# Performance work log

Measured on AMD Instinct MI355X. Metric: run time of the kernel, lower is better.

Reference implementation:

```python
import jax, jax.numpy as jnp
import numpy as np

IN_DIM, K, D, ITERS, EPS = 512, 8, 128, 3, 1e-8
LN_EPS = 1e-5

def _ln(x, g, b):
    m = jnp.mean(x, axis=-1, keepdims=True)
    v = jnp.var(x, axis=-1, keepdims=True)
    return (x - m) * jax.lax.rsqrt(v + LN_EPS) * g + b

def setup_inputs() -> dict:
    key = jax.random.key(0)
    ks = jax.random.split(key, 16)
    B, C, H, W = 64, IN_DIM, 32, 32
    s = lambda fan: 1.0 / np.sqrt(fan)
    inp = {
        'x': jax.random.normal(ks[0], (B, C, H, W), jnp.float32),
        'noise': jax.random.normal(ks[1], (B, K, D), jnp.float32),
        'slot_mu': jax.random.normal(ks[2], (1, K, D), jnp.float32) * 0.02,
        'slot_log_sigma': jnp.zeros((1, K, D), jnp.float32),
        'Wp': jax.random.uniform(ks[3], (IN_DIM, D), jnp.float32, -s(IN_DIM), s(IN_DIM)),
        'bp': jnp.zeros((D,), jnp.float32),
        'g_in': jnp.ones((D,), jnp.float32), 'b_in': jnp.zeros((D,), jnp.float32),
        'Wq': jax.random.uniform(ks[4], (D, D), jnp.float32, -s(D), s(D)),
        'bq': jnp.zeros((D,), jnp.float32),
        'Wk': jax.random.uniform(ks[5], (D, D), jnp.float32, -s(D), s(D)),
        'bk': jnp.zeros((D,), jnp.float32),
        'Wv': jax.random.uniform(ks[6], (D, D), jnp.float32, -s(D), s(D)),
        'bv': jnp.zeros((D,), jnp.float32),
        'W_ih': jax.random.uniform(ks[7], (3 * D, D), jnp.float32, -s(D), s(D)),
        'W_hh': jax.random.uniform(ks[8], (3 * D, D), jnp.float32, -s(D), s(D)),
        'b_ih': jax.random.uniform(ks[9], (3 * D,), jnp.float32, -s(D), s(D)),
        'b_hh': jax.random.uniform(ks[10], (3 * D,), jnp.float32, -s(D), s(D)),
        'W1': jax.random.uniform(ks[11], (D, 2 * D), jnp.float32, -s(D), s(D)),
        'b1': jnp.zeros((2 * D,), jnp.float32),
        'W2': jax.random.uniform(ks[12], (2 * D, D), jnp.float32, -s(2 * D), s(2 * D)),
        'b2': jnp.zeros((D,), jnp.float32),
        'g_slots': jnp.ones((D,), jnp.float32), 'b_slots': jnp.zeros((D,), jnp.float32),
        'g_mlp': jnp.ones((D,), jnp.float32), 'b_mlp': jnp.zeros((D,), jnp.float32),
    }
    return inp

def reference(x, noise, slot_mu, slot_log_sigma, Wp, bp, g_in, b_in,
              Wq, bq, Wk, bk, Wv, bv, W_ih, W_hh, b_ih, b_hh,
              W1, b1, W2, b2, g_slots, b_slots, g_mlp, b_mlp):
    B, C, H, W = x.shape
    N = H * W
    scale = D ** -0.5
    x_flat = x.reshape(B, C, N).transpose(0, 2, 1)          # [B,N,C]
    inputs = _ln(x_flat @ Wp + bp, g_in, b_in)              # [B,N,D]
    slots = slot_mu + jnp.exp(slot_log_sigma) * noise       # [B,K,D]
    k = inputs @ Wk + bk                                    # k/v are loop-invariant
    v = inputs @ Wv + bv
    attn = None
    for _ in range(ITERS):
        slots_prev = slots
        q = _ln(slots, g_slots, b_slots) @ Wq + bq          # [B,K,D]
        logits = jnp.einsum('bkd,bnd->bkn', q, k) * scale
        attn = jax.nn.softmax(logits, axis=1)               # softmax over slots
        attn_norm = attn / (jnp.sum(attn, axis=-1, keepdims=True) + EPS)
        updates = jnp.einsum('bkn,bnd->bkd', attn_norm, v)  # [B,K,D]
        # GRUCell (PyTorch gate order r,z,n)
        u2 = updates.reshape(B * K, D)
        h = slots_prev.reshape(B * K, D)
        gx = u2 @ W_ih.T + b_ih
        gh = h @ W_hh.T + b_hh
        xr, xz, xn = jnp.split(gx, 3, axis=-1)
        hr, hz, hn = jnp.split(gh, 3, axis=-1)
        r = jax.nn.sigmoid(xr + hr)
        z = jax.nn.sigmoid(xz + hz)
        n = jnp.tanh(xn + r * hn)
        slots = ((1.0 - z) * n + z * h).reshape(B, K, D)
        hmid = jax.nn.gelu(_ln(slots, g_mlp, b_mlp) @ W1 + b1, approximate=False)
        slots = slots + hmid @ W2 + b2
    return slots, attn
```

## Files before the change

kernel.cpp:

```cpp
#include <hip/hip_runtime.h>
#include <hip/hip_bf16.h>
#include <math.h>

#define B_ 64
#define C_ 512
#define N_ 1024
#define D_ 128
#define K_ 8

typedef __attribute__((ext_vector_type(8))) short bf16x8;
typedef __attribute__((ext_vector_type(4))) float f32x4;
typedef unsigned short ushort_t;

__device__ __forceinline__ unsigned short f2bs(float f) {
    union { __hip_bfloat16 h; unsigned short s; } u;
    u.h = __float2bfloat16(f);
    return u.s;
}
__device__ __forceinline__ float bs2f(unsigned short s) {
    union { unsigned int u; float f; } v;
    v.u = ((unsigned int)s) << 16;
    return v.f;
}
__device__ __forceinline__ float sigmoidf_(float x) { return 1.0f / (1.0f + expf(-x)); }
__device__ __forceinline__ float gelu_exact(float x) {
    return 0.5f * x * (1.0f + erff(x * 0.7071067811865476f));
}

__global__ __launch_bounds__(256) void prep_init(
    const float* __restrict__ Wp, const float* __restrict__ Wk,
    const float* __restrict__ Wv, const float* __restrict__ W_ih,
    const float* __restrict__ W_hh,
    const float* __restrict__ noise, const float* __restrict__ mu,
    const float* __restrict__ lsig,
    const float* __restrict__ g_slots, const float* __restrict__ b_slots,
    const float* __restrict__ Wq, const float* __restrict__ bq,
    ushort_t* __restrict__ WpT, ushort_t* __restrict__ WkT,
    ushort_t* __restrict__ WvT, float* __restrict__ WTih,
    float* __restrict__ WThh,
    float* __restrict__ slots, float* __restrict__ qbuf)
{
    __shared__ float sl2[2][128];
    __shared__ float tt2[2][128];
    __shared__ float mrs2[2][2];
    const int t = threadIdx.x;

    if (blockIdx.x < 256) {
        int tid = blockIdx.x * 256 + t;
        {
            int c = tid >> 7, d = tid & 127;
            WpT[d * 512 + c] = f2bs(Wp[tid]);
        }
        if (tid < 16384) {
            int c = tid >> 7, d = tid & 127;
            WkT[d * 128 + c] = f2bs(Wk[tid]);
            WvT[d * 128 + c] = f2bs(Wv[tid]);
        }
        if (tid < 49152) {
            int j = tid >> 7, c = tid & 127;
            WTih[c * 384 + j] = W_ih[tid];
            WThh[c * 384 + j] = W_hh[tid];
        }
        return;
    }

    const int lr = t >> 7, lt = t & 127;
    const int row = ((blockIdx.x - 256) << 1) | lr;
    const int b = row >> 3;
    const int kd = (row & 7) * 128 + lt;
    float sv = mu[kd] + expf(lsig[kd]) * noise[b * 1024 + kd];
    slots[(size_t)row * D_ + lt] = sv;
    sl2[lr][lt] = sv;
    __syncthreads();
    if (lt < 64) {
        float v0 = sl2[lr][lt], v1 = sl2[lr][lt + 64];
        float s = v0 + v1, s2 = v0 * v0 + v1 * v1;
        for (int off = 32; off > 0; off >>= 1) {
            s += __shfl_down(s, off, 64);
            s2 += __shfl_down(s2, off, 64);
        }
        if (lt == 0) {
            float mean = s * (1.f / 128.f);
            float var = s2 * (1.f / 128.f) - mean * mean;
            mrs2[lr][0] = mean; mrs2[lr][1] = rsqrtf(var + 1e-5f);
        }
    }
    __syncthreads();
    tt2[lr][lt] = (sl2[lr][lt] - mrs2[lr][0]) * mrs2[lr][1] * g_slots[lt] + b_slots[lt];
    __syncthreads();
    float a = bq[lt];
    for (int c = 0; c < 128; ++c) a = fmaf(tt2[lr][c], Wq[(size_t)c * D_ + lt], a);
    qbuf[(size_t)row * D_ + lt] = a;
}

__global__ __launch_bounds__(256) void proj_kv(
    const float* __restrict__ x, const ushort_t* __restrict__ WpT,
    const float* __restrict__ bp, const float* __restrict__ g_in,
    const float* __restrict__ b_in,
    const ushort_t* __restrict__ WkT, const float* __restrict__ bk,
    const ushort_t* __restrict__ WvT, const float* __restrict__ bv,
    ushort_t* __restrict__ kout, ushort_t* __restrict__ vout)
{
    __shared__ __align__(16) ushort_t Al[64 * 40];
    __shared__ __align__(16) ushort_t Bl[128 * 40];
    __shared__ __align__(16) ushort_t Bv2[128 * 40];
    __shared__ __align__(16) ushort_t A2[64 * 136];
    __shared__ float red[64][2][2];
    const int t = threadIdx.x;
    const int b = blockIdx.x >> 4;
    const int n0 = (blockIdx.x & 15) << 6;
    const int w = t >> 6, lane = t & 63;
    const int quad = lane >> 4, m = lane & 15;
    const int rowoff = (w >> 1) << 5;
    const int coloff = (w & 1) << 6;

    f32x4 acc[2][4];
#pragma unroll
    for (int r = 0; r < 2; ++r)
#pragma unroll
        for (int c = 0; c < 4; ++c) acc[r][c] = (f32x4){0.f, 0.f, 0.f, 0.f};

    const float* xb = x + (size_t)b * (C_ * N_);
    for (int c0 = 0; c0 < C_; c0 += 32) {
#pragma unroll
        for (int i = 0; i < 2; ++i) {
            int idx = t + (i << 8);
            int cc = idx >> 4;
            int nn4 = (idx & 15) << 2;
            float4 xv = *(const float4*)&xb[(size_t)(c0 + cc) * N_ + n0 + nn4];
            Al[(nn4    ) * 40 + cc] = f2bs(xv.x);
            Al[(nn4 + 1) * 40 + cc] = f2bs(xv.y);
            Al[(nn4 + 2) * 40 + cc] = f2bs(xv.z);
            Al[(nn4 + 3) * 40 + cc] = f2bs(xv.w);
        }
#pragma unroll
        for (int i = 0; i < 2; ++i) {
            int idx = t + (i << 8);
            int d = idx >> 2, seg = idx & 3;
            *(bf16x8*)&Bl[d * 40 + seg * 8] =
                *(const bf16x8*)&WpT[d * 512 + c0 + seg * 8];
        }
        __syncthreads();
        bf16x8 af[2], bfr[4];
#pragma unroll
        for (int r = 0; r < 2; ++r)
            af[r] = *(const bf16x8*)&Al[(rowoff + 16 * r + m) * 40 + quad * 8];
#pragma unroll
        for (int c = 0; c < 4; ++c)
            bfr[c] = *(const bf16x8*)&Bl[(coloff + 16 * c + m) * 40 + quad * 8];
#pragma unroll
        for (int r = 0; r < 2; ++r)
#pragma unroll
            for (int c = 0; c < 4; ++c)
                acc[r][c] = __builtin_amdgcn_mfma_f32_16x16x32_bf16(af[r], bfr[c], acc[r][c], 0, 0, 0);
        __syncthreads();
    }
    float gv[4], bvv[4], bpv[4];
#pragma unroll
    for (int c = 0; c < 4; ++c) {
        int col = coloff + 16 * c + m;
        bpv[c] = bp[col]; gv[c] = g_in[col]; bvv[c] = b_in[col];
    }
#pragma unroll
    for (int r = 0; r < 2; ++r)
#pragma unroll
        for (int c = 0; c < 4; ++c)
#pragma unroll
            for (int g = 0; g < 4; ++g) acc[r][c][g] += bpv[c];

#pragma unroll
    for (int r = 0; r < 2; ++r) {
#pragma unroll
        for (int g = 0; g < 4; ++g) {
            float s = 0.f, s2 = 0.f;
#pragma unroll
            for (int c = 0; c < 4; ++c) { float v = acc[r][c][g]; s += v; s2 += v * v; }
#pragma unroll
            for (int off = 1; off < 16; off <<= 1) {
                s += __shfl_xor(s, off, 64);
                s2 += __shfl_xor(s2, off, 64);
            }
            if (m == 0) {
                int row = rowoff + 16 * r + quad * 4 + g;
                red[row][w & 1][0] = s;
                red[row][w & 1][1] = s2;
            }
        }
    }
    __syncthreads();
#pragma unroll
    for (int r = 0; r < 2; ++r) {
#pragma unroll
        for (int g = 0; g < 4; ++g) {
            int row = rowoff + 16 * r + quad * 4 + g;
            float s = red[row][0][0] + red[row][1][0];
            float s2 = red[row][0][1] + red[row][1][1];
            float mean = s * (1.f / 128.f);
            float var = s2 * (1.f / 128.f) - mean * mean;
            float rs = rsqrtf(var + 1e-5f);
#pragma unroll
            for (int c = 0; c < 4; ++c) {
                int col = coloff + 16 * c + m;
                float v = (acc[r][c][g] - mean) * rs * gv[c] + bvv[c];
                A2[row * 136 + col] = f2bs(v);
            }
        }
    }

    const int is_v = w >> 1;
    const int rowoff2 = (w & 1) << 5;
    f32x4 acc2[2][8];
#pragma unroll
    for (int r = 0; r < 2; ++r)
#pragma unroll
        for (int c = 0; c < 8; ++c) acc2[r][c] = (f32x4){0.f, 0.f, 0.f, 0.f};

    for (int c0 = 0; c0 < D_; c0 += 32) {
#pragma unroll
        for (int i = 0; i < 2; ++i) {
            int idx = t + (i << 8);
            int d = idx >> 2, seg = idx & 3;
            *(bf16x8*)&Bl[d * 40 + seg * 8] =
                *(const bf16x8*)&WkT[d * 128 + c0 + seg * 8];
            *(bf16x8*)&Bv2[d * 40 + seg * 8] =
                *(const bf16x8*)&WvT[d * 128 + c0 + seg * 8];
        }
        __syncthreads();
        const ushort_t* Bsrc = is_v ? Bv2 : Bl;
        bf16x8 af[2], bfr[8];
#pragma unroll
        for (int r = 0; r < 2; ++r)
            af[r] = *(const bf16x8*)&A2[(rowoff2 + 16 * r + m) * 136 + c0 + quad * 8];
#pragma unroll
        for (int c = 0; c < 8; ++c)
            bfr[c] = *(const bf16x8*)&Bsrc[(16 * c + m) * 40 + quad * 8];
#pragma unroll
        for (int r = 0; r < 2; ++r)
#pragma unroll
            for (int c = 0; c < 8; ++c)
                acc2[r][c] = __builtin_amdgcn_mfma_f32_16x16x32_bf16(af[r], bfr[c], acc2[r][c], 0, 0, 0);
        __syncthreads();
    }
    const float* bias = is_v ? bv : bk;
    ushort_t* dst = is_v ? vout : kout;
    float bval[8];
#pragma unroll
    for (int c = 0; c < 8; ++c) bval[c] = bias[16 * c + m];
#pragma unroll
    for (int r = 0; r < 2; ++r) {
#pragma unroll
        for (int g = 0; g < 4; ++g) {
            int row = rowoff2 + 16 * r + quad * 4 + g;
            size_t base = ((size_t)b * N_ + n0 + row) * D_;
#pragma unroll
            for (int c = 0; c < 8; ++c)
                dst[base + 16 * c + m] = f2bs(acc2[r][c][g] + bval[c]);
        }
    }
}

__global__ __launch_bounds__(512, 2) void attn_pv(
    const ushort_t* __restrict__ kb, const ushort_t* __restrict__ vb,
    const float* __restrict__ qbuf,
    float* __restrict__ S_part, float* __restrict__ upd_part,
    float* __restrict__ out_attn, int last)
{
    __shared__ __align__(16) char scratch[69632];
    __shared__ __align__(16) float at8[8][264];
    __shared__ __align__(16) float qs[8][132];
    __shared__ float red2[4][8];
    ushort_t* kvt = (ushort_t*)scratch;
    float* red = (float*)scratch;

    const int t = threadIdx.x;
    const int qd = blockIdx.x, b = blockIdx.y;
    const int nbase = qd << 8;
    const int wv = t >> 6, lane = t & 63;
    const float SCALE = 0.08838834764831845f;

    for (int i = t; i < 1024; i += 512)
        qs[i >> 7][i & 127] = qbuf[(size_t)b * 1024 + i];
#pragma unroll
    for (int i = 0; i < 8; ++i) {
        int idx = t + (i << 9);
        int rr = idx >> 4, u8 = (idx & 15) << 3;
        *(bf16x8*)&kvt[rr * 136 + u8] =
            *(const bf16x8*)&kb[((size_t)b * N_ + nbase + rr) * D_ + u8];
    }
    __syncthreads();

    {
        const int rr = t & 255, kh = t >> 8;
        float acc[4] = {0.f, 0.f, 0.f, 0.f};
        for (int c0 = 0; c0 < 128; c0 += 8) {
            bf16x8 kr = *(const bf16x8*)&kvt[rr * 136 + c0];
            float kf[8];
#pragma unroll
            for (int j = 0; j < 8; ++j) kf[j] = bs2f((ushort_t)kr[j]);
#pragma unroll
            for (int kk = 0; kk < 4; ++kk) {
                f32x4 qa = *(const f32x4*)&qs[4 * kh + kk][c0];
                f32x4 qb = *(const f32x4*)&qs[4 * kh + kk][c0 + 4];
                acc[kk] = fmaf(qa[0], kf[0], acc[kk]);
                acc[kk] = fmaf(qa[1], kf[1], acc[kk]);
                acc[kk] = fmaf(qa[2], kf[2], acc[kk]);
                acc[kk] = fmaf(qa[3], kf[3], acc[kk]);
                acc[kk] = fmaf(qb[0], kf[4], acc[kk]);
                acc[kk] = fmaf(qb[1], kf[5], acc[kk]);
                acc[kk] = fmaf(qb[2], kf[6], acc[kk]);
                acc[kk] = fmaf(qb[3], kf[7], acc[kk]);
            }
        }
#pragma unroll
        for (int kk = 0; kk < 4; ++kk)
            at8[4 * kh + kk][rr] = acc[kk];
    }
    __syncthreads();

    if (t < 256) {
        float l[8];
#pragma unroll
        for (int k = 0; k < 8; ++k) l[k] = at8[k][t] * SCALE;
        float mx = l[0];
#pragma unroll
        for (int k = 1; k < 8; ++k) mx = fmaxf(mx, l[k]);
        float e[8], ssum = 0.f;
#pragma unroll
        for (int k = 0; k < 8; ++k) { e[k] = expf(l[k] - mx); ssum += e[k]; }
        float inv = 1.f / ssum;
        float p[8];
#pragma unroll
        for (int k = 0; k < 8; ++k) {
            p[k] = e[k] * inv;
            at8[k][t] = p[k];
            if (last) out_attn[((size_t)b * K_ + k) * N_ + nbase + t] = p[k];
        }
#pragma unroll
        for (int k = 0; k < 8; ++k) {
            float v = p[k];
            for (int off = 32; off > 0; off >>= 1) v += __shfl_down(v, off, 64);
            if (lane == 0) red2[wv][k] = v;
        }
    }
    __syncthreads();
    if (t < 8)
        S_part[((size_t)b * 4 + qd) * 8 + t] =
            red2[0][t] + red2[1][t] + red2[2][t] + red2[3][t];

#pragma unroll
    for (int i = 0; i < 8; ++i) {
        int idx = t + (i << 9);
        int rr = idx >> 4, u8 = (idx & 15) << 3;
        *(bf16x8*)&kvt[rr * 136 + u8] =
            *(const bf16x8*)&vb[((size_t)b * N_ + nbase + rr) * D_ + u8];
    }
    __syncthreads();

    {
        float acc[8][4];
#pragma unroll
        for (int k = 0; k < 8; ++k)
#pragma unroll
            for (int j = 0; j < 4; ++j) acc[k][j] = 0.f;
        const int d4 = (t & 31) * 4, s = t >> 5;
#pragma unroll
        for (int i2 = 0; i2 < 4; ++i2) {
            const int nn = (s << 4) + (i2 << 2);
            float vf[4][4];
#pragma unroll
            for (int i = 0; i < 4; ++i) {
                ushort4 v4 = *(const ushort4*)&kvt[(nn + i) * 136 + d4];
                vf[i][0] = bs2f(v4.x); vf[i][1] = bs2f(v4.y);
                vf[i][2] = bs2f(v4.z); vf[i][3] = bs2f(v4.w);
            }
#pragma unroll
            for (int k = 0; k < 8; ++k) {
                f32x4 a4 = *(const f32x4*)&at8[k][nn];
#pragma unroll
                for (int i = 0; i < 4; ++i) {
                    acc[k][0] = fmaf(a4[i], vf[i][0], acc[k][0]);
                    acc[k][1] = fmaf(a4[i], vf[i][1], acc[k][1]);
                    acc[k][2] = fmaf(a4[i], vf[i][2], acc[k][2]);
                    acc[k][3] = fmaf(a4[i], vf[i][3], acc[k][3]);
                }
            }
        }
        __syncthreads();
#pragma unroll
        for (int k = 0; k < 8; ++k)
#pragma unroll
            for (int j = 0; j < 4; ++j)
                acc[k][j] += __shfl_xor(acc[k][j], 32, 64);
        if (lane < 32) {
#pragma unroll
            for (int k = 0; k < 8; ++k)
#pragma unroll
                for (int j = 0; j < 4; ++j)
                    red[(wv * 8 + k) * 132 + lane * 4 + j] = acc[k][j];
        }
        __syncthreads();
        for (int i = t; i < 1024; i += 512) {
            int k = i >> 7, d = i & 127;
            float ssum = 0.f;
#pragma unroll
            for (int w = 0; w < 8; ++w) ssum += red[(w * 8 + k) * 132 + d];
            upd_part[((size_t)b * 4 + qd) * 1024 + i] = ssum;
        }
    }
}

__global__ __launch_bounds__(256) void gru_mlp_q(
    const float* __restrict__ upd_part, const float* __restrict__ S_part,
    float* __restrict__ slots,
    const float* __restrict__ WTih, const float* __restrict__ WThh,
    const float* __restrict__ b_ih, const float* __restrict__ b_hh,
    const float* __restrict__ W1, const float* __restrict__ b1,
    const float* __restrict__ W2, const float* __restrict__ b2,
    const float* __restrict__ g_mlp, const float* __restrict__ b_mlp,
    const float* __restrict__ g_slots, const float* __restrict__ b_slots,
    const float* __restrict__ Wq, const float* __restrict__ bq,
    float* __restrict__ qbuf,
    float* __restrict__ out_slots, int final_iter)
{
    __shared__ float u[128], h[128], gx[384], gh[384], sn[128], tt[128], hm[256];
    __shared__ float mrs[2];
    const int t = threadIdx.x;
    const int row = blockIdx.x;
    const int b = row >> 3, k = row & 7;
    if (t < 128) {
        size_t sb = (size_t)b * 4;
        float S = S_part[(sb + 0) * 8 + k] + S_part[(sb + 1) * 8 + k]
                + S_part[(sb + 2) * 8 + k] + S_part[(sb + 3) * 8 + k];
        float inv = 1.0f / (S + 1e-8f);
        int i = k * 128 + t;
        float up = upd_part[(sb + 0) * 1024 + i] + upd_part[(sb + 1) * 1024 + i]
                 + upd_part[(sb + 2) * 1024 + i] + upd_part[(sb + 3) * 1024 + i];
        u[t] = up * inv;
        h[t] = slots[(size_t)row * D_ + t];
    }
    __syncthreads();
    {
        int j = t;
        float ax = 0.f, ah = 0.f;
        for (int c = 0; c < 128; ++c) {
            float uc = u[c], hc = h[c];
            ax = fmaf(uc, WTih[(size_t)c * 384 + j], ax);
            ah = fmaf(hc, WThh[(size_t)c * 384 + j], ah);
        }
        gx[j] = ax + b_ih[j];
        gh[j] = ah + b_hh[j];
    }
    if (t < 128) {
        int j = 256 + t;
        float ax = 0.f, ah = 0.f;
        for (int c = 0; c < 128; ++c) {
            float uc = u[c], hc = h[c];
            ax = fmaf(uc, WTih[(size_t)c * 384 + j], ax);
            ah = fmaf(hc, WThh[(size_t)c * 384 + j], ah);
        }
        gx[j] = ax + b_ih[j];
        gh[j] = ah + b_hh[j];
    }
    __syncthreads();
    if (t < 128) {
        float r = sigmoidf_(gx[t] + gh[t]);
        float z = sigmoidf_(gx[t + 128] + gh[t + 128]);
        float nv = tanhf(gx[t + 256] + r * gh[t + 256]);
        sn[t] = (1.0f - z) * nv + z * h[t];
    }
    __syncthreads();
    if (t < 64) {
        float v0 = sn[t], v1 = sn[t + 64];
        float s = v0 + v1, s2 = v0 * v0 + v1 * v1;
        for (int off = 32; off > 0; off >>= 1) {
            s += __shfl_down(s, off, 64);
            s2 += __shfl_down(s2, off, 64);
        }
        if (t == 0) {
            float mean = s * (1.f / 128.f);
            float var = s2 * (1.f / 128.f) - mean * mean;
            mrs[0] = mean; mrs[1] = rsqrtf(var + 1e-5f);
        }
    }
    __syncthreads();
    if (t < 128) tt[t] = (sn[t] - mrs[0]) * mrs[1] * g_mlp[t] + b_mlp[t];
    __syncthreads();
    {
        float a = 0.f;
        for (int c = 0; c < 128; ++c) a = fmaf(tt[c], W1[(size_t)c * 256 + t], a);
        hm[t] = gelu_exact(a + b1[t]);
    }
    __syncthreads();
    if (t < 128) {
        float a = sn[t] + b2[t];
        for (int j = 0; j < 256; ++j) a = fmaf(hm[j], W2[(size_t)j * D_ + t], a);
        slots[(size_t)row * D_ + t] = a;
        if (final_iter) out_slots[(size_t)row * D_ + t] = a;
        u[t] = a;
    }
    __syncthreads();
    if (t < 64) {
        float v0 = u[t], v1 = u[t + 64];
        float s = v0 + v1, s2 = v0 * v0 + v1 * v1;
        for (int off = 32; off > 0; off >>= 1) {
            s += __shfl_down(s, off, 64);
            s2 += __shfl_down(s2, off, 64);
        }
        if (t == 0) {
            float mean = s * (1.f / 128.f);
            float var = s2 * (1.f / 128.f) - mean * mean;
            mrs[0] = mean; mrs[1] = rsqrtf(var + 1e-5f);
        }
    }
    __syncthreads();
    if (t < 128) tt[t] = (u[t] - mrs[0]) * mrs[1] * g_slots[t] + b_slots[t];
    __syncthreads();
    if (!final_iter && t < 128) {
        float a = bq[t];
        for (int c = 0; c < 128; ++c) a = fmaf(tt[c], Wq[(size_t)c * D_ + t], a);
        qbuf[(size_t)row * D_ + t] = a;
    }
}

extern "C" void kernel_launch(void* const* d_in, const int* in_sizes, int n_in,
                              void* d_out, int out_size, void* d_ws, size_t ws_size,
                              hipStream_t stream) {
    const float* x       = (const float*)d_in[0];
    const float* noise   = (const float*)d_in[1];
    const float* slot_mu = (const float*)d_in[2];
    const float* slot_ls = (const float*)d_in[3];
    const float* Wp      = (const float*)d_in[4];
    const float* bp      = (const float*)d_in[5];
    const float* g_in    = (const float*)d_in[6];
    const float* b_in    = (const float*)d_in[7];
    const float* Wq      = (const float*)d_in[8];
    const float* bq      = (const float*)d_in[9];
    const float* Wk      = (const float*)d_in[10];
    const float* bk      = (const float*)d_in[11];
    const float* Wv      = (const float*)d_in[12];
    const float* bv      = (const float*)d_in[13];
    const float* W_ih    = (const float*)d_in[14];
    const float* W_hh    = (const float*)d_in[15];
    const float* b_ih    = (const float*)d_in[16];
    const float* b_hh    = (const float*)d_in[17];
    const float* W1      = (const float*)d_in[18];
    const float* b1      = (const float*)d_in[19];
    const float* W2      = (const float*)d_in[20];
    const float* b2      = (const float*)d_in[21];
    const float* g_slots = (const float*)d_in[22];
    const float* b_slots = (const float*)d_in[23];
    const float* g_mlp   = (const float*)d_in[24];
    const float* b_mlp   = (const float*)d_in[25];

    float* out_slots = (float*)d_out;
    float* out_attn  = (float*)d_out + 65536;

    float* wsf = (float*)d_ws;
    ushort_t* kb = (ushort_t*)(wsf + 4194304);
    ushort_t* vb = (ushort_t*)(wsf + 8388608);
    float* slots    = wsf + 12582912;
    float* qbuf     = wsf + 12648448;
    float* upd_part = wsf + 12713984;
    float* S_part   = wsf + 12976128;
    ushort_t* WpT = (ushort_t*)(wsf + 13304320);
    ushort_t* WkT = (ushort_t*)(wsf + 13337088);
    ushort_t* WvT = (ushort_t*)(wsf + 13345280);
    float* WTih = wsf + 13353472;
    float* WThh = wsf + 13402624;

    prep_init<<<dim3(512), dim3(256), 0, stream>>>(
        Wp, Wk, Wv, W_ih, W_hh, noise, slot_mu, slot_ls,
        g_slots, b_slots, Wq, bq,
        WpT, WkT, WvT, WTih, WThh, slots, qbuf);
    proj_kv<<<dim3(1024), dim3(256), 0, stream>>>(
        x, WpT, bp, g_in, b_in, WkT, bk, WvT, bv, kb, vb);

    for (int it = 0; it < 3; ++it) {
        int last = (it == 2) ? 1 : 0;
        attn_pv<<<dim3(4, 64), dim3(512), 0, stream>>>(
            kb, vb, qbuf, S_part, upd_part, out_attn, last);
        gru_mlp_q<<<dim3(512), dim3(256), 0, stream>>>(
            upd_part, S_part, slots, WTih, WThh, b_ih, b_hh,
            W1, b1, W2, b2, g_mlp, b_mlp, g_slots, b_slots,
            Wq, bq, qbuf, out_slots, last);
    }
}
```

Before: 396.1 us.

## Load projection operands directly from global and XOR-swizzle K/V shared tiles

```diff
diff --git a/kernel.cpp b/kernel.cpp
--- a/kernel.cpp
+++ b/kernel.cpp
@@ -101,7 +101,6 @@
     const ushort_t* __restrict__ WvT, const float* __restrict__ bv,
     ushort_t* __restrict__ kout, ushort_t* __restrict__ vout)
 {
-    __shared__ __align__(16) ushort_t Al[64 * 40];
     __shared__ __align__(16) ushort_t Bl[128 * 40];
     __shared__ __align__(16) ushort_t Bv2[128 * 40];
     __shared__ __align__(16) ushort_t A2[64 * 136];
@@ -122,38 +121,24 @@
 
     const float* xb = x + (size_t)b * (C_ * N_);
     for (int c0 = 0; c0 < C_; c0 += 32) {
-#pragma unroll
-        for (int i = 0; i < 2; ++i) {
-            int idx = t + (i << 8);
-            int cc = idx >> 4;
-            int nn4 = (idx & 15) << 2;
-            float4 xv = *(const float4*)&xb[(size_t)(c0 + cc) * N_ + n0 + nn4];
-            Al[(nn4    ) * 40 + cc] = f2bs(xv.x);
-            Al[(nn4 + 1) * 40 + cc] = f2bs(xv.y);
-            Al[(nn4 + 2) * 40 + cc] = f2bs(xv.z);
-            Al[(nn4 + 3) * 40 + cc] = f2bs(xv.w);
-        }
-#pragma unroll
-        for (int i = 0; i < 2; ++i) {
-            int idx = t + (i << 8);
-            int d = idx >> 2, seg = idx & 3;
-            *(bf16x8*)&Bl[d * 40 + seg * 8] =
-                *(const bf16x8*)&WpT[d * 512 + c0 + seg * 8];
-        }
-        __syncthreads();
         bf16x8 af[2], bfr[4];
 #pragma unroll
-        for (int r = 0; r < 2; ++r)
-            af[r] = *(const bf16x8*)&Al[(rowoff + 16 * r + m) * 40 + quad * 8];
+        for (int r = 0; r < 2; ++r) {
+            union { ushort_t u[8]; bf16x8 v; } pk;
+            const int row = n0 + rowoff + 16 * r + m;
+#pragma unroll
+            for (int j = 0; j < 8; ++j)
+                pk.u[j] = f2bs(xb[(size_t)(c0 + quad * 8 + j) * N_ + row]);
+            af[r] = pk.v;
+        }
 #pragma unroll
         for (int c = 0; c < 4; ++c)
-            bfr[c] = *(const bf16x8*)&Bl[(coloff + 16 * c + m) * 40 + quad * 8];
+            bfr[c] = *(const bf16x8*)&WpT[(size_t)(coloff + 16 * c + m) * 512 + c0 + quad * 8];
 #pragma unroll
         for (int r = 0; r < 2; ++r)
 #pragma unroll
             for (int c = 0; c < 4; ++c)
                 acc[r][c] = __builtin_amdgcn_mfma_f32_16x16x32_bf16(af[r], bfr[c], acc[r][c], 0, 0, 0);
-        __syncthreads();
     }
     float gv[4], bvv[4], bpv[4];
 #pragma unroll
@@ -284,7 +269,8 @@
     for (int i = 0; i < 8; ++i) {
         int idx = t + (i << 9);
         int rr = idx >> 4, u8 = (idx & 15) << 3;
-        *(bf16x8*)&kvt[rr * 136 + u8] =
+        int su8 = u8 ^ ((rr & 15) << 3);
+        *(bf16x8*)&kvt[rr * 128 + su8] =
             *(const bf16x8*)&kb[((size_t)b * N_ + nbase + rr) * D_ + u8];
     }
     __syncthreads();
@@ -293,7 +279,7 @@
         const int rr = t & 255, kh = t >> 8;
         float acc[4] = {0.f, 0.f, 0.f, 0.f};
         for (int c0 = 0; c0 < 128; c0 += 8) {
-            bf16x8 kr = *(const bf16x8*)&kvt[rr * 136 + c0];
+            bf16x8 kr = *(const bf16x8*)&kvt[rr * 128 + (c0 ^ ((rr & 15) << 3))];
             float kf[8];
 #pragma unroll
             for (int j = 0; j < 8; ++j) kf[j] = bs2f((ushort_t)kr[j]);
@@ -351,7 +337,8 @@
     for (int i = 0; i < 8; ++i) {
         int idx = t + (i << 9);
         int rr = idx >> 4, u8 = (idx & 15) << 3;
-        *(bf16x8*)&kvt[rr * 136 + u8] =
+        int su8 = u8 ^ ((rr & 15) << 3);
+        *(bf16x8*)&kvt[rr * 128 + su8] =
             *(const bf16x8*)&vb[((size_t)b * N_ + nbase + rr) * D_ + u8];
     }
     __syncthreads();
@@ -369,7 +356,9 @@
             float vf[4][4];
 #pragma unroll
             for (int i = 0; i < 4; ++i) {
-                ushort4 v4 = *(const ushort4*)&kvt[(nn + i) * 136 + d4];
+                int row = nn + i;
+                int scol = (d4 & 7) | ((d4 & 0x78) ^ ((row & 15) << 3));
+                ushort4 v4 = *(const ushort4*)&kvt[row * 128 + scol];
                 vf[i][0] = bs2f(v4.x); vf[i][1] = bs2f(v4.y);
                 vf[i][2] = bs2f(v4.z); vf[i][3] = bs2f(v4.w);
             }
```

Result: slower. 412.1 us (+4.0%).
